# Optimization experiments

Hardware: AMD Instinct MI355X
Metric: run time of the kernel (lower is better)

## Reference

```python
import jax, jax.numpy as jnp
import numpy as np

B, N, D, K = 32, 1024, 768, 512

def setup_inputs() -> dict:
    key = jax.random.key(0)
    k1, k2 = jax.random.split(key)
    img_feat_map = jax.random.normal(k1, (B, N, D), dtype=jnp.float32)
    codebook = jax.random.normal(k2, (K, D), dtype=jnp.float32)
    return {"img_feat_map": img_feat_map, "codebook": codebook}

def reference(img_feat_map, codebook):
    # squared L2 distances between each token and each codebook vector
    x_sq = jnp.sum(img_feat_map ** 2, axis=2, keepdims=True)          # [B,N,1]
    c_sq = jnp.sum(codebook ** 2, axis=1)[None, None, :]              # [1,1,K]
    dot = jnp.einsum('bnd,kd->bnk', img_feat_map, codebook)           # [B,N,K]
    distances = x_sq + c_sq - 2.0 * dot                               # [B,N,K]
    soft_assignments = jax.nn.softmax(-distances, axis=2)             # [B,N,K]
    # aggregate tokens per codebook slot
    aggregated = jnp.einsum('bnk,bnd->bkd', soft_assignments, img_feat_map)  # [B,K,D]
    return aggregated
```

## Files before the change

kernel.cpp:

```cpp
#include <hip/hip_runtime.h>
#include <math.h>

#define BB 32
#define NN 1024
#define DD 768
#define KK 512
#define MM (BB * NN)

typedef _Float16 half8 __attribute__((ext_vector_type(8)));
typedef _Float16 half4 __attribute__((ext_vector_type(4)));
typedef float floatx4 __attribute__((ext_vector_type(4)));

__device__ __forceinline__ void load_lds16(const void* g, void* l) {
    __builtin_amdgcn_global_load_lds(
        (const __attribute__((address_space(1))) unsigned int*)g,
        (__attribute__((address_space(3))) unsigned int*)l, 16, 0, 0);
}

__global__ __launch_bounds__(256) void cast_f32_f16(const float* __restrict__ src,
                                                    _Float16* __restrict__ dst,
                                                    int n8) {
    int i = blockIdx.x * 256 + threadIdx.x;
    if (i >= n8) return;
    float4 a = ((const float4*)src)[2 * i];
    float4 b = ((const float4*)src)[2 * i + 1];
    half8 h;
    h[0] = (_Float16)a.x; h[1] = (_Float16)a.y; h[2] = (_Float16)a.z; h[3] = (_Float16)a.w;
    h[4] = (_Float16)b.x; h[5] = (_Float16)b.y; h[6] = (_Float16)b.z; h[7] = (_Float16)b.w;
    ((half8*)dst)[i] = h;
}

__global__ __launch_bounds__(256) void csq_kernel(const float* __restrict__ cb,
                                                  float* __restrict__ csq) {
    int k = blockIdx.x;
    const float* row = cb + (size_t)k * DD;
    float s = 0.f;
    for (int d = threadIdx.x; d < DD; d += 256) {
        float v = row[d];
        s += v * v;
    }
    #pragma unroll
    for (int off = 32; off > 0; off >>= 1) s += __shfl_down(s, off);
    __shared__ float sm[4];
    int lane = threadIdx.x & 63, wid = threadIdx.x >> 6;
    if (lane == 0) sm[wid] = s;
    __syncthreads();
    if (threadIdx.x == 0) csq[k] = sm[0] + sm[1] + sm[2] + sm[3];
}

__global__ __launch_bounds__(512, 4) void fused_logits_softmax(
    const float* __restrict__ X,
    const _Float16* __restrict__ Cbh,
    const float* __restrict__ csq,
    _Float16* __restrict__ St)
{
    __shared__ _Float16 Cs[2][512][32];
    __shared__ _Float16 Xs[2][64][32];
    __shared__ float redbuf[8][64];
    __shared__ float gred[64];

    const int t = threadIdx.x;
    const int w = t >> 6;
    const int lane = t & 63;
    const int l15 = lane & 15;
    const int quad = lane >> 4;
    const int wk = w * 64;
    const int gm0 = blockIdx.x * 64;

    const int qs = (quad ^ ((l15 >> 1) & 3)) * 8;

    float cs[4];
    #pragma unroll
    for (int ki = 0; ki < 4; ki++) cs[ki] = csq[wk + ki * 16 + l15];

    floatx4 acc[4][4] = {};

    const int cr = t >> 2;
    const int cq = (t & 3) ^ ((t >> 3) & 3);
    const float* xsrc = X + (size_t)(gm0 + cr) * DD + cq * 8;

    float4 xa, xb;
    if (t < 256) { xa = *(const float4*)xsrc; xb = *(const float4*)(xsrc + 4); }

    #pragma unroll
    for (int c = 0; c < 4; c++)
        load_lds16(Cbh + (size_t)(c * 128 + cr) * DD + cq * 8,
                   (_Float16*)Cs[0] + (c * 512 + t) * 8);
    if (t < 256) {
        half8 h;
        h[0] = (_Float16)xa.x; h[1] = (_Float16)xa.y; h[2] = (_Float16)xa.z; h[3] = (_Float16)xa.w;
        h[4] = (_Float16)xb.x; h[5] = (_Float16)xb.y; h[6] = (_Float16)xb.z; h[7] = (_Float16)xb.w;
        *(half8*)&Xs[0][cr][(t & 3) * 8] = h;
        xa = *(const float4*)(xsrc + 32);
        xb = *(const float4*)(xsrc + 36);
    }
    __syncthreads();

    int cur = 0;
    for (int it = 0; it < 24; ++it) {
        if (it + 1 < 24) {
            const int d0n = (it + 1) * 32;
            #pragma unroll
            for (int c = 0; c < 4; c++)
                load_lds16(Cbh + (size_t)(c * 128 + cr) * DD + d0n + cq * 8,
                           (_Float16*)Cs[cur ^ 1] + (c * 512 + t) * 8);
            if (t < 256) {
                half8 h;
                h[0] = (_Float16)xa.x; h[1] = (_Float16)xa.y; h[2] = (_Float16)xa.z; h[3] = (_Float16)xa.w;
                h[4] = (_Float16)xb.x; h[5] = (_Float16)xb.y; h[6] = (_Float16)xb.z; h[7] = (_Float16)xb.w;
                *(half8*)&Xs[cur ^ 1][cr][(t & 3) * 8] = h;
                if (it + 2 < 24) {
                    xa = *(const float4*)(xsrc + (it + 2) * 32);
                    xb = *(const float4*)(xsrc + (it + 2) * 32 + 4);
                }
            }
        }
        half8 af[4], bf[4];
        #pragma unroll
        for (int mi = 0; mi < 4; mi++) af[mi] = *(half8*)&Xs[cur][mi * 16 + l15][qs];
        #pragma unroll
        for (int ki = 0; ki < 4; ki++) bf[ki] = *(half8*)&Cs[cur][wk + ki * 16 + l15][qs];
        #pragma unroll
        for (int mi = 0; mi < 4; mi++)
            #pragma unroll
            for (int ki = 0; ki < 4; ki++)
                acc[mi][ki] = __builtin_amdgcn_mfma_f32_16x16x32_f16(af[mi], bf[ki], acc[mi][ki], 0, 0, 0);
        if (it + 1 < 24) { __syncthreads(); cur ^= 1; }
    }

    float pmax[4][4];
    #pragma unroll
    for (int mi = 0; mi < 4; mi++)
        #pragma unroll
        for (int r = 0; r < 4; r++) {
            float m = -1e30f;
            #pragma unroll
            for (int ki = 0; ki < 4; ki++)
                m = fmaxf(m, 2.f * acc[mi][ki][r] - cs[ki]);
            pmax[mi][r] = m;
        }
    #pragma unroll
    for (int off = 1; off < 16; off <<= 1)
        #pragma unroll
        for (int mi = 0; mi < 4; mi++)
            #pragma unroll
            for (int r = 0; r < 4; r++)
                pmax[mi][r] = fmaxf(pmax[mi][r], __shfl_xor(pmax[mi][r], off));
    if (l15 == 0) {
        #pragma unroll
        for (int mi = 0; mi < 4; mi++)
            #pragma unroll
            for (int r = 0; r < 4; r++)
                redbuf[w][mi * 16 + quad * 4 + r] = pmax[mi][r];
    }
    __syncthreads();
    if (t < 64) {
        float g = redbuf[0][t];
        #pragma unroll
        for (int wv = 1; wv < 8; wv++) g = fmaxf(g, redbuf[wv][t]);
        gred[t] = g;
    }
    __syncthreads();
    float gmax[4][4];
    #pragma unroll
    for (int mi = 0; mi < 4; mi++)
        #pragma unroll
        for (int r = 0; r < 4; r++)
            gmax[mi][r] = gred[mi * 16 + quad * 4 + r];

    float psum[4][4] = {};
    #pragma unroll
    for (int mi = 0; mi < 4; mi++)
        #pragma unroll
        for (int ki = 0; ki < 4; ki++) {
            floatx4 e;
            #pragma unroll
            for (int r = 0; r < 4; r++) {
                e[r] = __expf(2.f * acc[mi][ki][r] - cs[ki] - gmax[mi][r]);
                psum[mi][r] += e[r];
            }
            acc[mi][ki] = e;
        }
    #pragma unroll
    for (int off = 1; off < 16; off <<= 1)
        #pragma unroll
        for (int mi = 0; mi < 4; mi++)
            #pragma unroll
            for (int r = 0; r < 4; r++)
                psum[mi][r] += __shfl_xor(psum[mi][r], off);
    if (l15 == 0) {
        #pragma unroll
        for (int mi = 0; mi < 4; mi++)
            #pragma unroll
            for (int r = 0; r < 4; r++)
                redbuf[w][mi * 16 + quad * 4 + r] = psum[mi][r];
    }
    __syncthreads();
    if (t < 64) {
        float s = redbuf[0][t];
        #pragma unroll
        for (int wv = 1; wv < 8; wv++) s += redbuf[wv][t];
        gred[t] = 1.f / s;
    }
    __syncthreads();
    float ginv[4][4];
    #pragma unroll
    for (int mi = 0; mi < 4; mi++)
        #pragma unroll
        for (int r = 0; r < 4; r++)
            ginv[mi][r] = gred[mi * 16 + quad * 4 + r];

    const int b = gm0 >> 10;
    const int n0 = gm0 & 1023;
    #pragma unroll
    for (int mi = 0; mi < 4; mi++)
        #pragma unroll
        for (int ki = 0; ki < 4; ki++) {
            half4 s4;
            #pragma unroll
            for (int r = 0; r < 4; r++)
                s4[r] = (_Float16)(acc[mi][ki][r] * ginv[mi][r]);
            int k = wk + ki * 16 + l15;
            *(half4*)&St[((size_t)b * KK + k) * NN + n0 + mi * 16 + quad * 4] = s4;
        }
}

__global__ __launch_bounds__(256) void transpose_xt(const float* __restrict__ X,
                                                    _Float16* __restrict__ Xt) {
    const int n0 = blockIdx.x * 64;
    const int d0 = blockIdx.y * 32;
    const int b = blockIdx.z;
    __shared__ _Float16 Ls[64][40];
    const int t = threadIdx.x;
    const int r = t >> 2, c8 = (t & 3) * 8;
    const float* src = X + ((size_t)(b << 10) + n0 + r) * DD + d0 + c8;
    float4 f0 = *(const float4*)src;
    float4 f1 = *(const float4*)(src + 4);
    half8 h;
    h[0] = (_Float16)f0.x; h[1] = (_Float16)f0.y; h[2] = (_Float16)f0.z; h[3] = (_Float16)f0.w;
    h[4] = (_Float16)f1.x; h[5] = (_Float16)f1.y; h[6] = (_Float16)f1.z; h[7] = (_Float16)f1.w;
    *(half8*)&Ls[r][c8] = h;
    __syncthreads();
    const int dr = t >> 3;
    const int nc = (t & 7) * 8;
    half8 o;
    #pragma unroll
    for (int j = 0; j < 8; j++) o[j] = Ls[nc + j][dr];
    *(half8*)&Xt[((size_t)b * DD + d0 + dr) * NN + n0 + nc] = o;
}

__global__ __launch_bounds__(256, 4) void gemm2_mfma(const _Float16* __restrict__ St,
                                                     const _Float16* __restrict__ Xt,
                                                     float* __restrict__ out) {
    __shared__ _Float16 As[2][128][32];
    __shared__ _Float16 Bs[2][128][32];

    const int d0 = blockIdx.x * 128;
    const int k0 = blockIdx.y * 128;
    const int b = blockIdx.z;
    const int t = threadIdx.x;
    const int wave = t >> 6;
    const int lane = t & 63;
    const int wm = (wave >> 1) * 64;
    const int wn = (wave & 1) * 64;
    const int l15 = lane & 15;
    const int quad = lane >> 4;
    const int qs = (quad ^ ((l15 >> 1) & 3)) * 8;

    const int cr = t >> 2;
    const int cq = (t & 3) ^ ((t >> 3) & 3);

    floatx4 acc[4][4] = {};

    const _Float16* Abase = St + ((size_t)b * KK + k0) * NN;
    const _Float16* Bbase = Xt + ((size_t)b * DD + d0) * NN;

    #pragma unroll
    for (int c = 0; c < 2; c++) {
        load_lds16(Abase + (size_t)(c * 64 + cr) * NN + cq * 8,
                   (_Float16*)As[0] + (c * 256 + t) * 8);
        load_lds16(Bbase + (size_t)(c * 64 + cr) * NN + cq * 8,
                   (_Float16*)Bs[0] + (c * 256 + t) * 8);
    }
    __syncthreads();

    int cur = 0;
    for (int it = 0; it < 32; ++it) {
        if (it + 1 < 32) {
            const int n0 = (it + 1) * 32;
            #pragma unroll
            for (int c = 0; c < 2; c++) {
                load_lds16(Abase + (size_t)(c * 64 + cr) * NN + n0 + cq * 8,
                           (_Float16*)As[cur ^ 1] + (c * 256 + t) * 8);
                load_lds16(Bbase + (size_t)(c * 64 + cr) * NN + n0 + cq * 8,
                           (_Float16*)Bs[cur ^ 1] + (c * 256 + t) * 8);
            }
        }
        half8 af[4], bf[4];
        #pragma unroll
        for (int i = 0; i < 4; i++) af[i] = *(half8*)&As[cur][wm + i * 16 + l15][qs];
        #pragma unroll
        for (int i = 0; i < 4; i++) bf[i] = *(half8*)&Bs[cur][wn + i * 16 + l15][qs];
        #pragma unroll
        for (int mi = 0; mi < 4; mi++)
            #pragma unroll
            for (int ni = 0; ni < 4; ni++)
                acc[mi][ni] = __builtin_amdgcn_mfma_f32_16x16x32_f16(af[mi], bf[ni], acc[mi][ni], 0, 0, 0);
        if (it + 1 < 32) { __syncthreads(); cur ^= 1; }
    }

    #pragma unroll
    for (int ni = 0; ni < 4; ni++) {
        #pragma unroll
        for (int mi = 0; mi < 4; mi++) {
            int k = k0 + wm + mi * 16 + quad * 4;
            int d = d0 + wn + ni * 16 + l15;
            float* op = out + ((size_t)b * KK + k) * DD + d;
            floatx4 a = acc[mi][ni];
            op[0 * DD] = a[0];
            op[1 * DD] = a[1];
            op[2 * DD] = a[2];
            op[3 * DD] = a[3];
        }
    }
}

extern "C" void kernel_launch(void* const* d_in, const int* in_sizes, int n_in,
                              void* d_out, int out_size, void* d_ws, size_t ws_size,
                              hipStream_t stream) {
    const float* x  = (const float*)d_in[0];
    const float* cb = (const float*)d_in[1];
    float* out = (float*)d_out;

    char* ws = (char*)d_ws;
    float*    csq = (float*)ws;
    _Float16* Cbh = (_Float16*)(ws + 4096);
    _Float16* Xt  = (_Float16*)(ws + 4096 + 786432);
    _Float16* St  = (_Float16*)(ws + 4096 + 786432 + 50331648);

    cast_f32_f16<<<(KK * DD / 8 + 255) / 256, 256, 0, stream>>>(cb, Cbh, KK * DD / 8);
    csq_kernel<<<KK, 256, 0, stream>>>(cb, csq);

    fused_logits_softmax<<<MM / 64, 512, 0, stream>>>(x, Cbh, csq, St);

    transpose_xt<<<dim3(NN / 64, DD / 32, BB), 256, 0, stream>>>(x, Xt);

    gemm2_mfma<<<dim3(DD / 128, KK / 128, BB), 256, 0, stream>>>(St, Xt, out);
}
```

Baseline: 292.3 us.

## Deepen prefetch pipelines with partial vmcnt waits in both GEMM kernels

In the distance GEMM, all threads now load the fp32 X tile with float4 loads kept two stages ahead in registers. Barriers become explicit s_waitcnt plus s_barrier, so loads still in flight are not drained every iteration. The aggregation GEMM moves from double to triple buffered LDS, prefetching two K-steps ahead with vmcnt(4) waits, and lowers launch bounds to 3 blocks per CU to fit the extra LDS. The aim is to hide global load latency behind MFMA work, at the cost of occupancy, more registers, and fragile hand-counted waitcnt logic.

```diff
diff --git a/kernel.cpp b/kernel.cpp
--- a/kernel.cpp
+++ b/kernel.cpp
@@ -15,6 +15,11 @@
     __builtin_amdgcn_global_load_lds(
         (const __attribute__((address_space(1))) unsigned int*)g,
         (__attribute__((address_space(3))) unsigned int*)l, 16, 0, 0);
+}
+
+__device__ __forceinline__ void mem_fence_sched() {
+    asm volatile("" ::: "memory");
+    __builtin_amdgcn_sched_barrier(0);
 }
 
 __global__ __launch_bounds__(256) void cast_f32_f16(const float* __restrict__ src,
@@ -77,55 +82,62 @@
 
     const int cr = t >> 2;
     const int cq = (t & 3) ^ ((t >> 3) & 3);
-    const float* xsrc = X + (size_t)(gm0 + cr) * DD + cq * 8;
-
-    float4 xa, xb;
-    if (t < 256) { xa = *(const float4*)xsrc; xb = *(const float4*)(xsrc + 4); }
+
+    const int xr = t >> 3;
+    const int xc = (t & 7) * 4;
+    const int xq = (t & 7) >> 1;
+    const int xoff = xr * 32 + (xq ^ ((xr >> 1) & 3)) * 8 + (xc & 7);
+    const float* xsrc = X + (size_t)(gm0 + xr) * DD + xc;
 
     #pragma unroll
     for (int c = 0; c < 4; c++)
         load_lds16(Cbh + (size_t)(c * 128 + cr) * DD + cq * 8,
                    (_Float16*)Cs[0] + (c * 512 + t) * 8);
-    if (t < 256) {
-        half8 h;
-        h[0] = (_Float16)xa.x; h[1] = (_Float16)xa.y; h[2] = (_Float16)xa.z; h[3] = (_Float16)xa.w;
-        h[4] = (_Float16)xb.x; h[5] = (_Float16)xb.y; h[6] = (_Float16)xb.z; h[7] = (_Float16)xb.w;
-        *(half8*)&Xs[0][cr][(t & 3) * 8] = h;
-        xa = *(const float4*)(xsrc + 32);
-        xb = *(const float4*)(xsrc + 36);
-    }
-    __syncthreads();
-
-    int cur = 0;
+    float4 xv0 = *(const float4*)xsrc;
+    float4 xn1 = *(const float4*)(xsrc + 32);
+    float4 xn2 = *(const float4*)(xsrc + 64);
+    {
+        half4 h;
+        h[0] = (_Float16)xv0.x; h[1] = (_Float16)xv0.y;
+        h[2] = (_Float16)xv0.z; h[3] = (_Float16)xv0.w;
+        *(half4*)((_Float16*)Xs[0] + xoff) = h;
+    }
+    __syncthreads();
+
     for (int it = 0; it < 24; ++it) {
-        if (it + 1 < 24) {
+        const int cur = it & 1;
+        if (it < 23) {
+            half4 h;
+            h[0] = (_Float16)xn1.x; h[1] = (_Float16)xn1.y;
+            h[2] = (_Float16)xn1.z; h[3] = (_Float16)xn1.w;
+            *(half4*)((_Float16*)Xs[cur ^ 1] + xoff) = h;
             const int d0n = (it + 1) * 32;
             #pragma unroll
             for (int c = 0; c < 4; c++)
                 load_lds16(Cbh + (size_t)(c * 128 + cr) * DD + d0n + cq * 8,
                            (_Float16*)Cs[cur ^ 1] + (c * 512 + t) * 8);
-            if (t < 256) {
-                half8 h;
-                h[0] = (_Float16)xa.x; h[1] = (_Float16)xa.y; h[2] = (_Float16)xa.z; h[3] = (_Float16)xa.w;
-                h[4] = (_Float16)xb.x; h[5] = (_Float16)xb.y; h[6] = (_Float16)xb.z; h[7] = (_Float16)xb.w;
-                *(half8*)&Xs[cur ^ 1][cr][(t & 3) * 8] = h;
-                if (it + 2 < 24) {
-                    xa = *(const float4*)(xsrc + (it + 2) * 32);
-                    xb = *(const float4*)(xsrc + (it + 2) * 32 + 4);
-                }
-            }
+            mem_fence_sched();
+            xn1 = xn2;
+            if (it < 21) xn2 = *(const float4*)(xsrc + (it + 3) * 32);
         }
         half8 af[4], bf[4];
         #pragma unroll
-        for (int mi = 0; mi < 4; mi++) af[mi] = *(half8*)&Xs[cur][mi * 16 + l15][qs];
-        #pragma unroll
-        for (int ki = 0; ki < 4; ki++) bf[ki] = *(half8*)&Cs[cur][wk + ki * 16 + l15][qs];
+        for (int mi = 0; mi < 4; mi++)
+            af[mi] = *(half8*)((_Float16*)Xs[cur] + (mi * 16 + l15) * 32 + qs);
+        #pragma unroll
+        for (int ki = 0; ki < 4; ki++)
+            bf[ki] = *(half8*)((_Float16*)Cs[cur] + (wk + ki * 16 + l15) * 32 + qs);
         #pragma unroll
         for (int mi = 0; mi < 4; mi++)
             #pragma unroll
             for (int ki = 0; ki < 4; ki++)
                 acc[mi][ki] = __builtin_amdgcn_mfma_f32_16x16x32_f16(af[mi], bf[ki], acc[mi][ki], 0, 0, 0);
-        if (it + 1 < 24) { __syncthreads(); cur ^= 1; }
+        if (it < 23) {
+            if (it < 21) asm volatile("s_waitcnt vmcnt(1) lgkmcnt(0)" ::: "memory");
+            else         asm volatile("s_waitcnt vmcnt(0) lgkmcnt(0)" ::: "memory");
+            __builtin_amdgcn_s_barrier();
+            __builtin_amdgcn_sched_barrier(0);
+        }
     }
 
     float pmax[4][4];
@@ -249,11 +261,11 @@
     *(half8*)&Xt[((size_t)b * DD + d0 + dr) * NN + n0 + nc] = o;
 }
 
-__global__ __launch_bounds__(256, 4) void gemm2_mfma(const _Float16* __restrict__ St,
+__global__ __launch_bounds__(256, 3) void gemm2_mfma(const _Float16* __restrict__ St,
                                                      const _Float16* __restrict__ Xt,
                                                      float* __restrict__ out) {
-    __shared__ _Float16 As[2][128][32];
-    __shared__ _Float16 Bs[2][128][32];
+    __shared__ _Float16 As[3][128][32];
+    __shared__ _Float16 Bs[3][128][32];
 
     const int d0 = blockIdx.x * 128;
     const int k0 = blockIdx.y * 128;
@@ -282,31 +294,54 @@
         load_lds16(Bbase + (size_t)(c * 64 + cr) * NN + cq * 8,
                    (_Float16*)Bs[0] + (c * 256 + t) * 8);
     }
-    __syncthreads();
-
-    int cur = 0;
+    mem_fence_sched();
+    #pragma unroll
+    for (int c = 0; c < 2; c++) {
+        load_lds16(Abase + (size_t)(c * 64 + cr) * NN + 32 + cq * 8,
+                   (_Float16*)As[1] + (c * 256 + t) * 8);
+        load_lds16(Bbase + (size_t)(c * 64 + cr) * NN + 32 + cq * 8,
+                   (_Float16*)Bs[1] + (c * 256 + t) * 8);
+    }
+    asm volatile("s_waitcnt vmcnt(4)" ::: "memory");
+    __builtin_amdgcn_s_barrier();
+    __builtin_amdgcn_sched_barrier(0);
+
+    int ic = 0, js = 2;
     for (int it = 0; it < 32; ++it) {
-        if (it + 1 < 32) {
-            const int n0 = (it + 1) * 32;
+        if (it < 30) {
+            const int n0s = (it + 2) * 32;
+            _Float16* Ad = (_Float16*)As[js];
+            _Float16* Bd = (_Float16*)Bs[js];
             #pragma unroll
             for (int c = 0; c < 2; c++) {
-                load_lds16(Abase + (size_t)(c * 64 + cr) * NN + n0 + cq * 8,
-                           (_Float16*)As[cur ^ 1] + (c * 256 + t) * 8);
-                load_lds16(Bbase + (size_t)(c * 64 + cr) * NN + n0 + cq * 8,
-                           (_Float16*)Bs[cur ^ 1] + (c * 256 + t) * 8);
+                load_lds16(Abase + (size_t)(c * 64 + cr) * NN + n0s + cq * 8,
+                           Ad + (c * 256 + t) * 8);
+                load_lds16(Bbase + (size_t)(c * 64 + cr) * NN + n0s + cq * 8,
+                           Bd + (c * 256 + t) * 8);
             }
         }
+        const _Float16* Ar = (const _Float16*)As[ic];
+        const _Float16* Br = (const _Float16*)Bs[ic];
         half8 af[4], bf[4];
         #pragma unroll
-        for (int i = 0; i < 4; i++) af[i] = *(half8*)&As[cur][wm + i * 16 + l15][qs];
-        #pragma unroll
-        for (int i = 0; i < 4; i++) bf[i] = *(half8*)&Bs[cur][wn + i * 16 + l15][qs];
+        for (int i = 0; i < 4; i++)
+            af[i] = *(const half8*)(Ar + (wm + i * 16 + l15) * 32 + qs);
+        #pragma unroll
+        for (int i = 0; i < 4; i++)
+            bf[i] = *(const half8*)(Br + (wn + i * 16 + l15) * 32 + qs);
         #pragma unroll
         for (int mi = 0; mi < 4; mi++)
             #pragma unroll
             for (int ni = 0; ni < 4; ni++)
                 acc[mi][ni] = __builtin_amdgcn_mfma_f32_16x16x32_f16(af[mi], bf[ni], acc[mi][ni], 0, 0, 0);
-        if (it + 1 < 32) { __syncthreads(); cur ^= 1; }
+        if (it < 31) {
+            if (it < 30) asm volatile("s_waitcnt vmcnt(4) lgkmcnt(0)" ::: "memory");
+            else         asm volatile("s_waitcnt vmcnt(0) lgkmcnt(0)" ::: "memory");
+            __builtin_amdgcn_s_barrier();
+            __builtin_amdgcn_sched_barrier(0);
+        }
+        ic = (ic == 2) ? 0 : ic + 1;
+        js = (js == 2) ? 0 : js + 1;
     }
 
     #pragma unroll
```

Result: slower. 302.9 us (+3.6%).

## Fuse X transpose into logits kernel and merge codebook prep kernels

Applied to the files above, without the earlier changes.

The fp16 transposed copy of X is now written from the LDS tile already staged inside the logits/softmax kernel, which removes the separate transpose kernel and its second full read of X from global memory. The codebook cast and squared-norm kernels are merged into one launch. In exchange, each logits iteration does extra LDS reads and scattered half4 global stores, which may interfere with the MFMA loop. The codebook cast now uses scalar stores.

```diff
diff --git a/kernel.cpp b/kernel.cpp
--- a/kernel.cpp
+++ b/kernel.cpp
@@ -17,27 +17,17 @@
         (__attribute__((address_space(3))) unsigned int*)l, 16, 0, 0);
 }
 
-__global__ __launch_bounds__(256) void cast_f32_f16(const float* __restrict__ src,
-                                                    _Float16* __restrict__ dst,
-                                                    int n8) {
-    int i = blockIdx.x * 256 + threadIdx.x;
-    if (i >= n8) return;
-    float4 a = ((const float4*)src)[2 * i];
-    float4 b = ((const float4*)src)[2 * i + 1];
-    half8 h;
-    h[0] = (_Float16)a.x; h[1] = (_Float16)a.y; h[2] = (_Float16)a.z; h[3] = (_Float16)a.w;
-    h[4] = (_Float16)b.x; h[5] = (_Float16)b.y; h[6] = (_Float16)b.z; h[7] = (_Float16)b.w;
-    ((half8*)dst)[i] = h;
-}
-
-__global__ __launch_bounds__(256) void csq_kernel(const float* __restrict__ cb,
-                                                  float* __restrict__ csq) {
+__global__ __launch_bounds__(256) void prep_codebook(const float* __restrict__ cb,
+                                                     _Float16* __restrict__ Cbh,
+                                                     float* __restrict__ csq) {
     int k = blockIdx.x;
     const float* row = cb + (size_t)k * DD;
+    _Float16* orow = Cbh + (size_t)k * DD;
     float s = 0.f;
     for (int d = threadIdx.x; d < DD; d += 256) {
         float v = row[d];
         s += v * v;
+        orow[d] = (_Float16)v;
     }
     #pragma unroll
     for (int off = 32; off > 0; off >>= 1) s += __shfl_down(s, off);
@@ -52,7 +42,8 @@
     const float* __restrict__ X,
     const _Float16* __restrict__ Cbh,
     const float* __restrict__ csq,
-    _Float16* __restrict__ St)
+    _Float16* __restrict__ St,
+    _Float16* __restrict__ Xt)
 {
     __shared__ _Float16 Cs[2][512][32];
     __shared__ _Float16 Xs[2][64][32];
@@ -66,6 +57,8 @@
     const int quad = lane >> 4;
     const int wk = w * 64;
     const int gm0 = blockIdx.x * 64;
+    const int b = gm0 >> 10;
+    const int n0 = gm0 & 1023;
 
     const int qs = (quad ^ ((l15 >> 1) & 3)) * 8;
 
@@ -78,6 +71,9 @@
     const int cr = t >> 2;
     const int cq = (t & 3) ^ ((t >> 3) & 3);
     const float* xsrc = X + (size_t)(gm0 + cr) * DD + cq * 8;
+
+    const int tdr = t >> 4;
+    const int tn4 = (t & 15) * 4;
 
     float4 xa, xb;
     if (t < 256) { xa = *(const float4*)xsrc; xb = *(const float4*)(xsrc + 4); }
@@ -98,8 +94,9 @@
 
     int cur = 0;
     for (int it = 0; it < 24; ++it) {
+        const int d0 = it * 32;
         if (it + 1 < 24) {
-            const int d0n = (it + 1) * 32;
+            const int d0n = d0 + 32;
             #pragma unroll
             for (int c = 0; c < 4; c++)
                 load_lds16(Cbh + (size_t)(c * 128 + cr) * DD + d0n + cq * 8,
@@ -115,11 +112,23 @@
                 }
             }
         }
+        {
+            half4 xo;
+            #pragma unroll
+            for (int j = 0; j < 4; j++) {
+                int n = tn4 + j;
+                xo[j] = *((const _Float16*)Xs[cur] + n * 32 +
+                          (((tdr >> 3) ^ ((n >> 1) & 3)) << 3) + (tdr & 7));
+            }
+            *(half4*)&Xt[((size_t)b * DD + d0 + tdr) * NN + n0 + tn4] = xo;
+        }
         half8 af[4], bf[4];
         #pragma unroll
-        for (int mi = 0; mi < 4; mi++) af[mi] = *(half8*)&Xs[cur][mi * 16 + l15][qs];
-        #pragma unroll
-        for (int ki = 0; ki < 4; ki++) bf[ki] = *(half8*)&Cs[cur][wk + ki * 16 + l15][qs];
+        for (int mi = 0; mi < 4; mi++)
+            af[mi] = *(half8*)((_Float16*)Xs[cur] + (mi * 16 + l15) * 32 + qs);
+        #pragma unroll
+        for (int ki = 0; ki < 4; ki++)
+            bf[ki] = *(half8*)((_Float16*)Cs[cur] + (wk + ki * 16 + l15) * 32 + qs);
         #pragma unroll
         for (int mi = 0; mi < 4; mi++)
             #pragma unroll
@@ -210,8 +219,6 @@
         for (int r = 0; r < 4; r++)
             ginv[mi][r] = gred[mi * 16 + quad * 4 + r];
 
-    const int b = gm0 >> 10;
-    const int n0 = gm0 & 1023;
     #pragma unroll
     for (int mi = 0; mi < 4; mi++)
         #pragma unroll
@@ -223,30 +230,6 @@
             int k = wk + ki * 16 + l15;
             *(half4*)&St[((size_t)b * KK + k) * NN + n0 + mi * 16 + quad * 4] = s4;
         }
-}
-
-__global__ __launch_bounds__(256) void transpose_xt(const float* __restrict__ X,
-                                                    _Float16* __restrict__ Xt) {
-    const int n0 = blockIdx.x * 64;
-    const int d0 = blockIdx.y * 32;
-    const int b = blockIdx.z;
-    __shared__ _Float16 Ls[64][40];
-    const int t = threadIdx.x;
-    const int r = t >> 2, c8 = (t & 3) * 8;
-    const float* src = X + ((size_t)(b << 10) + n0 + r) * DD + d0 + c8;
-    float4 f0 = *(const float4*)src;
-    float4 f1 = *(const float4*)(src + 4);
-    half8 h;
-    h[0] = (_Float16)f0.x; h[1] = (_Float16)f0.y; h[2] = (_Float16)f0.z; h[3] = (_Float16)f0.w;
-    h[4] = (_Float16)f1.x; h[5] = (_Float16)f1.y; h[6] = (_Float16)f1.z; h[7] = (_Float16)f1.w;
-    *(half8*)&Ls[r][c8] = h;
-    __syncthreads();
-    const int dr = t >> 3;
-    const int nc = (t & 7) * 8;
-    half8 o;
-    #pragma unroll
-    for (int j = 0; j < 8; j++) o[j] = Ls[nc + j][dr];
-    *(half8*)&Xt[((size_t)b * DD + d0 + dr) * NN + n0 + nc] = o;
 }
 
 __global__ __launch_bounds__(256, 4) void gemm2_mfma(const _Float16* __restrict__ St,
@@ -338,12 +321,9 @@
     _Float16* Xt  = (_Float16*)(ws + 4096 + 786432);
     _Float16* St  = (_Float16*)(ws + 4096 + 786432 + 50331648);
 
-    cast_f32_f16<<<(KK * DD / 8 + 255) / 256, 256, 0, stream>>>(cb, Cbh, KK * DD / 8);
-    csq_kernel<<<KK, 256, 0, stream>>>(cb, csq);
-
-    fused_logits_softmax<<<MM / 64, 512, 0, stream>>>(x, Cbh, csq, St);
-
-    transpose_xt<<<dim3(NN / 64, DD / 32, BB), 256, 0, stream>>>(x, Xt);
+    prep_codebook<<<KK, 256, 0, stream>>>(cb, Cbh, csq);
+
+    fused_logits_softmax<<<MM / 64, 512, 0, stream>>>(x, Cbh, csq, St, Xt);
 
     gemm2_mfma<<<dim3(DD / 128, KK / 128, BB), 256, 0, stream>>>(St, Xt, out);
 }
```

Result: faster. 274.4 us (-6.1%).
